# Kernel tuning notes

Hardware: AMD Instinct MI355X
Metric: run time of the kernel (lower is better)

The kernel has to match this reference:

```python
import jax, jax.numpy as jnp
import numpy as np

NEG_SLOPE = 0.2
NEG_INF = -1e9


def _gat_branch(x, src, dst, edge_type, t, W, a_src, a_dst, b):
    """Single-head PyG GATConv restricted (by masking) to edges with edge_type == t,
    with self-loops added (PyG default add_self_loops=True)."""
    N = x.shape[0]
    h = x @ W                                   # [N, out_dim]
    s = h @ a_src                               # [N] source attention term
    d = h @ a_dst                               # [N] destination attention term
    # real edges (masked by type)
    e_edge = jax.nn.leaky_relu(s[src] + d[dst], NEG_SLOPE)
    e_edge = jnp.where(edge_type == t, e_edge, NEG_INF)
    # self-loop edges i -> i
    e_self = jax.nn.leaky_relu(s + d, NEG_SLOPE)
    dst_all = jnp.concatenate([dst, jnp.arange(N)])          # [E+N]
    e_all = jnp.concatenate([e_edge, e_self])                 # [E+N]
    # softmax over incoming edges per destination node (segment softmax)
    m = jax.ops.segment_max(e_all, dst_all, num_segments=N)
    p = jnp.exp(e_all - m[dst_all])
    denom = jax.ops.segment_sum(p, dst_all, num_segments=N)
    alpha = p / denom[dst_all]                                 # [E+N]
    msg = jnp.concatenate([h[src], h], axis=0) * alpha[:, None]
    return jax.ops.segment_sum(msg, dst_all, num_segments=N) + b


def setup_inputs() -> dict:
    key = jax.random.key(0)
    ks = jax.random.split(key, 12)
    N, E, in_dim, out_dim = 100000, 1000000, 64, 64
    glorot = (6.0 / (in_dim + out_dim)) ** 0.5
    att = (6.0 / (1 + out_dim)) ** 0.5
    return {
        "x": jax.random.normal(ks[0], (N, in_dim), dtype=jnp.float32),
        "edge_index": jax.random.randint(ks[1], (2, E), 0, N),
        "edge_type": jax.random.randint(ks[2], (E,), 0, 2),
        "W_login": jax.random.uniform(ks[3], (in_dim, out_dim), jnp.float32, -glorot, glorot),
        "a_src_login": jax.random.uniform(ks[4], (out_dim,), jnp.float32, -att, att),
        "a_dst_login": jax.random.uniform(ks[5], (out_dim,), jnp.float32, -att, att),
        "b_login": jnp.zeros((out_dim,), jnp.float32),
        "W_exec": jax.random.uniform(ks[6], (in_dim, out_dim), jnp.float32, -glorot, glorot),
        "a_src_exec": jax.random.uniform(ks[7], (out_dim,), jnp.float32, -att, att),
        "a_dst_exec": jax.random.uniform(ks[8], (out_dim,), jnp.float32, -att, att),
        "b_exec": jnp.zeros((out_dim,), jnp.float32),
    }


def reference(x, edge_index, edge_type, W_login, a_src_login, a_dst_login, b_login,
              W_exec, a_src_exec, a_dst_exec, b_exec):
    src, dst = edge_index[0], edge_index[1]
    out = _gat_branch(x, src, dst, edge_type, 0, W_login, a_src_login, a_dst_login, b_login)
    out = out + _gat_branch(x, src, dst, edge_type, 1, W_exec, a_src_exec, a_dst_exec, b_exec)
    return out
```

## Files before the change

kernel.cpp:

```cpp
#include <hip/hip_runtime.h>

#define D 64
#define CAP 896
#define CNTB 512
#define GEMMB 768
#define BINCH 1600

typedef unsigned short u16;
typedef __attribute__((ext_vector_type(8))) __bf16 bf16x8;
typedef __attribute__((ext_vector_type(4))) float f32x4;

__device__ __forceinline__ float lrelu(float x) { return x > 0.f ? x : 0.2f * x; }
__device__ __forceinline__ u16 f2bf(float f) {
    unsigned u = __float_as_uint(f);
    return (u16)((u + 0x7fffu + ((u >> 16) & 1u)) >> 16);
}
__device__ __forceinline__ unsigned pack2(float lo, float hi) {
    return (unsigned)f2bf(lo) | ((unsigned)f2bf(hi) << 16);
}
__device__ __forceinline__ float blo(unsigned u) { return __uint_as_float(u << 16); }
__device__ __forceinline__ float bhi(unsigned u) { return __uint_as_float(u & 0xffff0000u); }

struct alignas(16) SG { u16 Xb[64][72]; float wsd[4][64]; };
struct SB { int cnt[BINCH]; };

__global__ __launch_bounds__(256) void k_wt(
    const float* __restrict__ W0, const float* __restrict__ as0, const float* __restrict__ ad0,
    const float* __restrict__ W1, const float* __restrict__ as1, const float* __restrict__ ad1,
    u16* __restrict__ Wt, float* __restrict__ wsd_g)
{
    const int tid = threadIdx.x;
    for (int i = tid; i < 4096; i += 256) {
        const int k = i >> 6, n = i & 63;
        Wt[(n << 6) + k]        = f2bf(W0[i]);
        Wt[4096 + (n << 6) + k] = f2bf(W1[i]);
    }
    const int k = tid & 63;
    const int v = tid >> 6;
    const float* Ws = (v < 2) ? W0 : W1;
    const float* av = (v == 0) ? as0 : (v == 1) ? ad0 : (v == 2) ? as1 : ad1;
    float q = 0.f;
    for (int n = 0; n < 64; ++n) q = fmaf(Ws[(k << 6) + n], av[n], q);
    wsd_g[(v << 6) + k] = q;
}

__global__ __launch_bounds__(256) void k_gc(
    const float* __restrict__ x,
    const u16* __restrict__ Wt, const float* __restrict__ wsd_g,
    u16* __restrict__ hb, float* __restrict__ s_tab, float* __restrict__ d_tab,
    int N, int ntiles,
    const int* __restrict__ dst, u16* __restrict__ cm, int E, int nbk, int Eseg)
{
    __shared__ union SM { SG g; SB bn; } sm;
    const int tid = threadIdx.x;

    if (blockIdx.x >= GEMMB) {
        int* cnt_l = sm.bn.cnt;
        const int blk = blockIdx.x - GEMMB;
        const long e0 = (long)blk * Eseg;
        const long e1 = min(e0 + (long)Eseg, (long)E);
        for (int base = 0; base < nbk; base += BINCH) {
            const int lim = min(BINCH, nbk - base);
            for (int i = tid; i < lim; i += 256) cnt_l[i] = 0;
            __syncthreads();
            long i = e0 + tid;
            for (; i + 256 * 7 < e1; i += 256 * 8) {
                int d8[8];
#pragma unroll
                for (int k = 0; k < 8; ++k) d8[k] = dst[i + 256 * k];
#pragma unroll
                for (int k = 0; k < 8; ++k) {
                    const int bb = (d8[k] >> 6) - base;
                    if ((unsigned)bb < (unsigned)lim) atomicAdd(&cnt_l[bb], 1);
                }
            }
            for (; i < e1; i += 256) {
                const int bb = (dst[i] >> 6) - base;
                if ((unsigned)bb < (unsigned)lim) atomicAdd(&cnt_l[bb], 1);
            }
            __syncthreads();
            for (int j = tid; j < lim; j += 256)
                cm[(size_t)(base + j) * CNTB + blk] = (u16)cnt_l[j];
            __syncthreads();
        }
        return;
    }

    auto& Xb  = sm.g.Xb;
    auto& wsd = sm.g.wsd;

    sm.g.wsd[tid >> 6][tid & 63] = wsd_g[tid];

    const int lane = tid & 63;
    const int nl = lane & 15, quad = lane >> 4;
    const int wv = tid >> 6;

    bf16x8 bfrag[2][4][2];
#pragma unroll
    for (int br = 0; br < 2; ++br)
#pragma unroll
        for (int t = 0; t < 4; ++t)
#pragma unroll
            for (int h = 0; h < 2; ++h)
                bfrag[br][t][h] = *(const bf16x8*)&Wt[((br << 12) | ((t * 16 + nl) << 6)) + h * 32 + quad * 8];

    __syncthreads();

    const int rstage = tid >> 2;
    const int kc = (tid & 3) << 4;

    for (int tile = blockIdx.x; tile < ntiles; tile += GEMMB) {
        const long n0 = (long)tile << 6;
        __syncthreads();
        {
            long row = n0 + rstage; if (row >= N) row = N - 1;
            const float4* xp = (const float4*)(x + row * D + kc);
            const float4 v0 = xp[0], v1 = xp[1], v2 = xp[2], v3 = xp[3];

            unsigned q[8];
            q[0] = pack2(v0.x, v0.y); q[1] = pack2(v0.z, v0.w);
            q[2] = pack2(v1.x, v1.y); q[3] = pack2(v1.z, v1.w);
            q[4] = pack2(v2.x, v2.y); q[5] = pack2(v2.z, v2.w);
            q[6] = pack2(v3.x, v3.y); q[7] = pack2(v3.z, v3.w);
            *(uint4*)&Xb[rstage][kc]     = make_uint4(q[0], q[1], q[2], q[3]);
            *(uint4*)&Xb[rstage][kc + 8] = make_uint4(q[4], q[5], q[6], q[7]);

            float ps[4];
#pragma unroll
            for (int v = 0; v < 4; ++v) {
                const float4* wp = (const float4*)&wsd[v][kc];
                const float4 wa = wp[0], wb = wp[1], wc = wp[2], wd = wp[3];
                float s = 0.f;
                s = fmaf(v0.x, wa.x, s); s = fmaf(v0.y, wa.y, s);
                s = fmaf(v0.z, wa.z, s); s = fmaf(v0.w, wa.w, s);
                s = fmaf(v1.x, wb.x, s); s = fmaf(v1.y, wb.y, s);
                s = fmaf(v1.z, wb.z, s); s = fmaf(v1.w, wb.w, s);
                s = fmaf(v2.x, wc.x, s); s = fmaf(v2.y, wc.y, s);
                s = fmaf(v2.z, wc.z, s); s = fmaf(v2.w, wc.w, s);
                s = fmaf(v3.x, wd.x, s); s = fmaf(v3.y, wd.y, s);
                s = fmaf(v3.z, wd.z, s); s = fmaf(v3.w, wd.w, s);
                ps[v] = s;
            }
#pragma unroll
            for (int v = 0; v < 4; ++v) {
                ps[v] += __shfl_xor(ps[v], 1, 64);
                ps[v] += __shfl_xor(ps[v], 2, 64);
            }
            const long rw = n0 + rstage;
            if ((tid & 3) == 0 && rw < N) {
                s_tab[(rw << 1)]     = ps[0]; d_tab[(rw << 1)]     = ps[1];
                s_tab[(rw << 1) | 1] = ps[2]; d_tab[(rw << 1) | 1] = ps[3];
            }
        }
        __syncthreads();

        const int rbase = wv << 4;
        const bf16x8 a0 = *(const bf16x8*)&Xb[rbase + nl][quad * 8];
        const bf16x8 a1 = *(const bf16x8*)&Xb[rbase + nl][32 + quad * 8];

        f32x4 acc[2][4];
#pragma unroll
        for (int br = 0; br < 2; ++br)
#pragma unroll
            for (int t = 0; t < 4; ++t) {
                f32x4 c = {0.f, 0.f, 0.f, 0.f};
                c = __builtin_amdgcn_mfma_f32_16x16x32_bf16(a0, bfrag[br][t][0], c, 0, 0, 0);
                c = __builtin_amdgcn_mfma_f32_16x16x32_bf16(a1, bfrag[br][t][1], c, 0, 0, 0);
                acc[br][t] = c;
            }

#pragma unroll
        for (int reg = 0; reg < 4; ++reg) {
            const long row = n0 + rbase + (quad << 2) + reg;
            if (row < N) {
#pragma unroll
                for (int br = 0; br < 2; ++br) {
                    uint2 v;
                    v.x = pack2(acc[br][0][reg], acc[br][1][reg]);
                    v.y = pack2(acc[br][2][reg], acc[br][3][reg]);
                    *(uint2*)(hb + (((row << 1) | br) << 6) + (nl << 2)) = v;
                }
            }
        }
    }
}

__global__ __launch_bounds__(256) void k_off(
    u16* __restrict__ cm, int* __restrict__ bktcnt, int nbk)
{
    const int lane = threadIdx.x & 63;
    const int j = blockIdx.x * 4 + (threadIdx.x >> 6);
    if (j >= nbk) return;

    const uint4 u = *(const uint4*)(cm + (size_t)j * CNTB + (lane << 3));
    int c[8] = { (int)(u.x & 0xffff), (int)(u.x >> 16),
                 (int)(u.y & 0xffff), (int)(u.y >> 16),
                 (int)(u.z & 0xffff), (int)(u.z >> 16),
                 (int)(u.w & 0xffff), (int)(u.w >> 16) };
    int e[8]; int run = 0;
#pragma unroll
    for (int k = 0; k < 8; ++k) { e[k] = run; run += c[k]; }
    int incl = run;
#pragma unroll
    for (int o = 1; o < 64; o <<= 1) {
        const int t = __shfl_up(incl, o, 64);
        if (lane >= o) incl += t;
    }
    const int excl = incl - run;
#pragma unroll
    for (int k = 0; k < 8; ++k) e[k] += excl;

    uint4 o4;
    o4.x = (unsigned)(e[0] & 0xffff) | ((unsigned)(e[1] & 0xffff) << 16);
    o4.y = (unsigned)(e[2] & 0xffff) | ((unsigned)(e[3] & 0xffff) << 16);
    o4.z = (unsigned)(e[4] & 0xffff) | ((unsigned)(e[5] & 0xffff) << 16);
    o4.w = (unsigned)(e[6] & 0xffff) | ((unsigned)(e[7] & 0xffff) << 16);
    *(uint4*)(cm + (size_t)j * CNTB + (lane << 3)) = o4;

    if (lane == 63) bktcnt[j] = incl;
}

__global__ __launch_bounds__(256) void k_emit(
    const int* __restrict__ src, const int* __restrict__ dst,
    const int* __restrict__ et, const u16* __restrict__ cm,
    unsigned* __restrict__ bkt, int E, int nbk, int Eseg)
{
    extern __shared__ int curl[];
    const int tid = threadIdx.x;
    const int blk = blockIdx.x;
    const long e0 = (long)blk * Eseg;
    const long e1 = min(e0 + (long)Eseg, (long)E);

    for (int base = 0; base < nbk; base += BINCH) {
        const int lim = min(BINCH, nbk - base);
        for (int i = tid; i < lim; i += 256)
            curl[i] = (int)cm[(size_t)(base + i) * CNTB + blk];
        __syncthreads();

        long i = e0 + tid;
        for (; i + 256 * 7 < e1; i += 256 * 8) {
            int d8[8], s8[8], t8[8];
#pragma unroll
            for (int k = 0; k < 8; ++k) d8[k] = dst[i + 256 * k];
#pragma unroll
            for (int k = 0; k < 8; ++k) s8[k] = src[i + 256 * k];
#pragma unroll
            for (int k = 0; k < 8; ++k) t8[k] = et[i + 256 * k];
#pragma unroll
            for (int k = 0; k < 8; ++k) {
                const int bb = (d8[k] >> 6) - base;
                if ((unsigned)bb < (unsigned)lim) {
                    const int slot = atomicAdd(&curl[bb], 1);
                    if (slot < CAP)
                        bkt[(long)(base + bb) * CAP + slot] =
                            ((unsigned)(d8[k] & 63) << 18) | ((unsigned)s8[k] << 1) | (unsigned)t8[k];
                }
            }
        }
        for (; i < e1; i += 256) {
            const int d = dst[i];
            const int bb = (d >> 6) - base;
            if ((unsigned)bb < (unsigned)lim) {
                const int slot = atomicAdd(&curl[bb], 1);
                if (slot < CAP)
                    bkt[(long)(base + bb) * CAP + slot] =
                        ((unsigned)(d & 63) << 18) | ((unsigned)src[i] << 1) | (unsigned)et[i];
            }
        }
        __syncthreads();
    }
}

__global__ __launch_bounds__(512) void k_proc(
    const int* __restrict__ bktcnt, const unsigned* __restrict__ bkt,
    const float* __restrict__ s_tab, const float* __restrict__ d_tab,
    const u16* __restrict__ hb,
    const float* __restrict__ b0, const float* __restrict__ b1,
    float* __restrict__ out, int N)
{
    __shared__ uint2 tok2[CAP + 128];
    __shared__ int   degl[64];
    __shared__ int   curl[64];
    __shared__ float den[128];
    __shared__ float dl[128];
    __shared__ float bsum[64];

    const int tid = threadIdx.x;
    const int b = blockIdx.x;
    const int lo = b << 6;
    const int cnt_nodes = min(64, N - lo);
    const int nb = min(bktcnt[b], CAP);

    if (tid < 64) {
        degl[tid] = (lo + tid < N) ? 2 : 0;
        bsum[tid] = b0[tid] + b1[tid];
    }
    if (tid < 128) {
        den[tid] = 0.f;
        const int n = lo + (tid >> 1);
        dl[tid] = (n < N) ? d_tab[(n << 1) | (tid & 1)] : 0.f;
    }
    __syncthreads();

    unsigned pr[2]; int ns = 0;
    for (int i = tid; i < nb; i += 512) {
        const unsigned p = bkt[(long)b * CAP + i];
        pr[ns++] = p;
        atomicAdd(&degl[(p >> 18) & 63], 1);
    }
    __syncthreads();
    if (tid < 64) {
        int v = degl[tid];
        const int orig = v;
#pragma unroll
        for (int o = 1; o < 64; o <<= 1) {
            const int u = __shfl_up(v, o, 64);
            if (tid >= o) v += u;
        }
        curl[tid] = v - orig;
    }
    __syncthreads();
    if (tid < 2 * cnt_nodes) {
        const int ni = tid >> 1;
        const int slot = atomicAdd(&curl[ni], 1);
        tok2[slot].x = ((unsigned)ni << 18) | ((unsigned)((lo + ni) << 1)) | (unsigned)(tid & 1);
    }
    for (int k = 0, i = tid; k < ns; i += 512, ++k) {
        const unsigned p = pr[k];
        const int slot = atomicAdd(&curl[(p >> 18) & 63], 1);
        tok2[slot].x = p;
    }
    __syncthreads();

    const int T = nb + (cnt_nodes << 1);
    for (int j = tid; j < T; j += 512) {
        const unsigned u = tok2[j].x;
        const int idx = (int)(((u >> 18) << 1) | (u & 1u));
        const float e = lrelu(s_tab[u & 0x3FFFFu] + dl[idx]);
        const float p = __expf(e);
        tok2[j].y = __float_as_uint(p);
        atomicAdd(&den[idx], p);
    }
    __syncthreads();

    const int lane = tid & 63;
    const int wave = tid >> 6;
    const int q = lane >> 4;
    const int cl = lane & 15;

    for (int ni = wave; ni < cnt_nodes; ni += 8) {
        const int cnt = degl[ni];
        const int off = curl[ni] - cnt;
        const float r0 = 1.f / den[(ni << 1)];
        const float r1 = 1.f / den[(ni << 1) | 1];

        float4 acc = {0.f, 0.f, 0.f, 0.f};
        const int nq = (cnt + 3) >> 2;
        int pp = 0;
        for (; pp + 1 < nq; pp += 2) {
            const int iA = (pp << 2) + q;
            const int iB = iA + 4;
            const uint2 eA = tok2[off + iA];
            const uint2 eB = tok2[off + (iB < cnt ? iB : cnt - 1)];
            const float aA = __uint_as_float(eA.y) * ((eA.x & 1u) ? r1 : r0);
            float aB = __uint_as_float(eB.y) * ((eB.x & 1u) ? r1 : r0);
            if (iB >= cnt) aB = 0.f;
            const uint2 uA = *(const uint2*)(hb + ((long)(eA.x & 0x3FFFFu) << 6) + (cl << 2));
            const uint2 uB = *(const uint2*)(hb + ((long)(eB.x & 0x3FFFFu) << 6) + (cl << 2));
            acc.x = fmaf(aA, blo(uA.x), acc.x);
            acc.y = fmaf(aA, bhi(uA.x), acc.y);
            acc.z = fmaf(aA, blo(uA.y), acc.z);
            acc.w = fmaf(aA, bhi(uA.y), acc.w);
            acc.x = fmaf(aB, blo(uB.x), acc.x);
            acc.y = fmaf(aB, bhi(uB.x), acc.y);
            acc.z = fmaf(aB, blo(uB.y), acc.z);
            acc.w = fmaf(aB, bhi(uB.y), acc.w);
        }
        if (pp < nq) {
            const int iA = (pp << 2) + q;
            const uint2 eA = tok2[off + (iA < cnt ? iA : cnt - 1)];
            float aA = __uint_as_float(eA.y) * ((eA.x & 1u) ? r1 : r0);
            if (iA >= cnt) aA = 0.f;
            const uint2 uA = *(const uint2*)(hb + ((long)(eA.x & 0x3FFFFu) << 6) + (cl << 2));
            acc.x = fmaf(aA, blo(uA.x), acc.x);
            acc.y = fmaf(aA, bhi(uA.x), acc.y);
            acc.z = fmaf(aA, blo(uA.y), acc.z);
            acc.w = fmaf(aA, bhi(uA.y), acc.w);
        }
        acc.x += __shfl_xor(acc.x, 16, 64);
        acc.y += __shfl_xor(acc.y, 16, 64);
        acc.z += __shfl_xor(acc.z, 16, 64);
        acc.w += __shfl_xor(acc.w, 16, 64);
        acc.x += __shfl_xor(acc.x, 32, 64);
        acc.y += __shfl_xor(acc.y, 32, 64);
        acc.z += __shfl_xor(acc.z, 32, 64);
        acc.w += __shfl_xor(acc.w, 32, 64);
        if (lane < 16) {
            float* op = out + ((long)(lo + ni) << 6);
            op[cl]      = acc.x + bsum[cl];
            op[16 + cl] = acc.y + bsum[16 + cl];
            op[32 + cl] = acc.z + bsum[32 + cl];
            op[48 + cl] = acc.w + bsum[48 + cl];
        }
    }
}

extern "C" void kernel_launch(void* const* d_in, const int* in_sizes, int n_in,
                              void* d_out, int out_size, void* d_ws, size_t ws_size,
                              hipStream_t stream) {
    const float* x   = (const float*)d_in[0];
    const int*   ei  = (const int*)d_in[1];
    const int*   et  = (const int*)d_in[2];
    const float* W0  = (const float*)d_in[3];
    const float* as0 = (const float*)d_in[4];
    const float* ad0 = (const float*)d_in[5];
    const float* b0  = (const float*)d_in[6];
    const float* W1  = (const float*)d_in[7];
    const float* as1 = (const float*)d_in[8];
    const float* ad1 = (const float*)d_in[9];
    const float* b1  = (const float*)d_in[10];
    float* out = (float*)d_out;

    const int N = in_sizes[0] / D;
    const int E = in_sizes[1] / 2;
    const int* src = ei;
    const int* dst = ei + E;

    const int nbk = (N + 63) >> 6;

    char* w = (char*)d_ws;
    auto carve = [&w](size_t bytes) {
        char* p = w;
        w += (bytes + 255) & ~(size_t)255;
        return p;
    };
    u16* hb       = (u16*)carve((size_t)2 * N * D * sizeof(u16));
    float* s_tab  = (float*)carve((size_t)2 * N * sizeof(float));
    float* d_tab  = (float*)carve((size_t)2 * N * sizeof(float));
    int* bktcnt   = (int*)carve((size_t)nbk * sizeof(int));
    unsigned* bkt = (unsigned*)carve((size_t)nbk * CAP * sizeof(unsigned));
    u16* cm       = (u16*)carve((size_t)nbk * CNTB * sizeof(u16));
    u16* Wt       = (u16*)carve((size_t)2 * 64 * 64 * sizeof(u16));
    float* wsd_g  = (float*)carve((size_t)4 * 64 * sizeof(float));

    const int ntiles = (N + 63) / 64;
    const int Eseg = (E + CNTB - 1) / CNTB;
    const int offb = (nbk + 3) / 4;

    k_wt<<<1, 256, 0, stream>>>(W0, as0, ad0, W1, as1, ad1, Wt, wsd_g);
    k_gc<<<GEMMB + CNTB, 256, 0, stream>>>(x, Wt, wsd_g,
                                           hb, s_tab, d_tab, N, ntiles,
                                           dst, cm, E, nbk, Eseg);
    k_off<<<offb, 256, 0, stream>>>(cm, bktcnt, nbk);
    k_emit<<<CNTB, 256, (size_t)BINCH * sizeof(int), stream>>>(
        src, dst, et, cm, bkt, E, nbk, Eseg);
    k_proc<<<nbk, 512, 0, stream>>>(bktcnt, bkt, s_tab, d_tab, hb, b0, b1, out, N);
}
```

Before: 185.0 us.

## Reschedule kernels: count first, overlap GEMM with bucket emit, prenormalize alphas

The weight-transpose work moves into the histogram-count kernel as an extra block, and the prefix-offset kernel now runs before the GEMM. The bucket-emit phase is then co-scheduled with the GEMM blocks in one launch, instead of the count phase sharing the launch with the GEMM. This removes one launch and overlaps the heavier scatter work with the dense matmul. In the aggregation kernel, the per-token alpha is multiplied by the reciprocal denominator in a shared-memory pass, so the inner loop no longer selects per branch. The trade-off is an extra sync and shared-memory pass per block, and the count kernel now runs alone without overlap.

```diff
diff --git a/kernel.cpp b/kernel.cpp
--- a/kernel.cpp
+++ b/kernel.cpp
@@ -22,65 +22,149 @@
 __device__ __forceinline__ float bhi(unsigned u) { return __uint_as_float(u & 0xffff0000u); }
 
 struct alignas(16) SG { u16 Xb[64][72]; float wsd[4][64]; };
-struct SB { int cnt[BINCH]; };
-
-__global__ __launch_bounds__(256) void k_wt(
+
+__global__ __launch_bounds__(256) void k_cnt(
+    const int* __restrict__ dst, u16* __restrict__ cm, int E, int nbk, int Eseg,
     const float* __restrict__ W0, const float* __restrict__ as0, const float* __restrict__ ad0,
     const float* __restrict__ W1, const float* __restrict__ as1, const float* __restrict__ ad1,
     u16* __restrict__ Wt, float* __restrict__ wsd_g)
 {
+    __shared__ int cnt_l[BINCH];
     const int tid = threadIdx.x;
-    for (int i = tid; i < 4096; i += 256) {
-        const int k = i >> 6, n = i & 63;
-        Wt[(n << 6) + k]        = f2bf(W0[i]);
-        Wt[4096 + (n << 6) + k] = f2bf(W1[i]);
-    }
-    const int k = tid & 63;
-    const int v = tid >> 6;
-    const float* Ws = (v < 2) ? W0 : W1;
-    const float* av = (v == 0) ? as0 : (v == 1) ? ad0 : (v == 2) ? as1 : ad1;
-    float q = 0.f;
-    for (int n = 0; n < 64; ++n) q = fmaf(Ws[(k << 6) + n], av[n], q);
-    wsd_g[(v << 6) + k] = q;
-}
-
-__global__ __launch_bounds__(256) void k_gc(
+
+    if (blockIdx.x >= CNTB) {
+        for (int i = tid; i < 4096; i += 256) {
+            const int k = i >> 6, n = i & 63;
+            Wt[(n << 6) + k]        = f2bf(W0[i]);
+            Wt[4096 + (n << 6) + k] = f2bf(W1[i]);
+        }
+        const int k = tid & 63;
+        const int v = tid >> 6;
+        const float* Ws = (v < 2) ? W0 : W1;
+        const float* av = (v == 0) ? as0 : (v == 1) ? ad0 : (v == 2) ? as1 : ad1;
+        float q = 0.f;
+        for (int n = 0; n < 64; ++n) q = fmaf(Ws[(k << 6) + n], av[n], q);
+        wsd_g[(v << 6) + k] = q;
+        return;
+    }
+
+    const int blk = blockIdx.x;
+    const long e0 = (long)blk * Eseg;
+    const long e1 = min(e0 + (long)Eseg, (long)E);
+    for (int base = 0; base < nbk; base += BINCH) {
+        const int lim = min(BINCH, nbk - base);
+        for (int i = tid; i < lim; i += 256) cnt_l[i] = 0;
+        __syncthreads();
+        long i = e0 + tid;
+        for (; i + 256 * 7 < e1; i += 256 * 8) {
+            int d8[8];
+#pragma unroll
+            for (int k = 0; k < 8; ++k) d8[k] = dst[i + 256 * k];
+#pragma unroll
+            for (int k = 0; k < 8; ++k) {
+                const int bb = (d8[k] >> 6) - base;
+                if ((unsigned)bb < (unsigned)lim) atomicAdd(&cnt_l[bb], 1);
+            }
+        }
+        for (; i < e1; i += 256) {
+            const int bb = (dst[i] >> 6) - base;
+            if ((unsigned)bb < (unsigned)lim) atomicAdd(&cnt_l[bb], 1);
+        }
+        __syncthreads();
+        for (int j = tid; j < lim; j += 256)
+            cm[(size_t)(base + j) * CNTB + blk] = (u16)cnt_l[j];
+        __syncthreads();
+    }
+}
+
+__global__ __launch_bounds__(256) void k_off(
+    u16* __restrict__ cm, int* __restrict__ bktcnt, int nbk)
+{
+    const int lane = threadIdx.x & 63;
+    const int j = blockIdx.x * 4 + (threadIdx.x >> 6);
+    if (j >= nbk) return;
+
+    const uint4 u = *(const uint4*)(cm + (size_t)j * CNTB + (lane << 3));
+    int c[8] = { (int)(u.x & 0xffff), (int)(u.x >> 16),
+                 (int)(u.y & 0xffff), (int)(u.y >> 16),
+                 (int)(u.z & 0xffff), (int)(u.z >> 16),
+                 (int)(u.w & 0xffff), (int)(u.w >> 16) };
+    int e[8]; int run = 0;
+#pragma unroll
+    for (int k = 0; k < 8; ++k) { e[k] = run; run += c[k]; }
+    int incl = run;
+#pragma unroll
+    for (int o = 1; o < 64; o <<= 1) {
+        const int t = __shfl_up(incl, o, 64);
+        if (lane >= o) incl += t;
+    }
+    const int excl = incl - run;
+#pragma unroll
+    for (int k = 0; k < 8; ++k) e[k] += excl;
+
+    uint4 o4;
+    o4.x = (unsigned)(e[0] & 0xffff) | ((unsigned)(e[1] & 0xffff) << 16);
+    o4.y = (unsigned)(e[2] & 0xffff) | ((unsigned)(e[3] & 0xffff) << 16);
+    o4.z = (unsigned)(e[4] & 0xffff) | ((unsigned)(e[5] & 0xffff) << 16);
+    o4.w = (unsigned)(e[6] & 0xffff) | ((unsigned)(e[7] & 0xffff) << 16);
+    *(uint4*)(cm + (size_t)j * CNTB + (lane << 3)) = o4;
+
+    if (lane == 63) bktcnt[j] = incl;
+}
+
+__global__ __launch_bounds__(256) void k_ge(
     const float* __restrict__ x,
     const u16* __restrict__ Wt, const float* __restrict__ wsd_g,
     u16* __restrict__ hb, float* __restrict__ s_tab, float* __restrict__ d_tab,
     int N, int ntiles,
-    const int* __restrict__ dst, u16* __restrict__ cm, int E, int nbk, int Eseg)
+    const int* __restrict__ src, const int* __restrict__ dst, const int* __restrict__ et,
+    const u16* __restrict__ cm, unsigned* __restrict__ bkt, int E, int nbk, int Eseg)
 {
-    __shared__ union SM { SG g; SB bn; } sm;
+    __shared__ union SM { SG g; int cnt[BINCH]; } sm;
     const int tid = threadIdx.x;
 
     if (blockIdx.x >= GEMMB) {
-        int* cnt_l = sm.bn.cnt;
+        int* curl = sm.cnt;
         const int blk = blockIdx.x - GEMMB;
         const long e0 = (long)blk * Eseg;
         const long e1 = min(e0 + (long)Eseg, (long)E);
+
         for (int base = 0; base < nbk; base += BINCH) {
             const int lim = min(BINCH, nbk - base);
-            for (int i = tid; i < lim; i += 256) cnt_l[i] = 0;
+            for (int i = tid; i < lim; i += 256)
+                curl[i] = (int)cm[(size_t)(base + i) * CNTB + blk];
             __syncthreads();
+
             long i = e0 + tid;
             for (; i + 256 * 7 < e1; i += 256 * 8) {
-                int d8[8];
+                int d8[8], s8[8], t8[8];
 #pragma unroll
                 for (int k = 0; k < 8; ++k) d8[k] = dst[i + 256 * k];
+#pragma unroll
+                for (int k = 0; k < 8; ++k) s8[k] = src[i + 256 * k];
+#pragma unroll
+                for (int k = 0; k < 8; ++k) t8[k] = et[i + 256 * k];
 #pragma unroll
                 for (int k = 0; k < 8; ++k) {
                     const int bb = (d8[k] >> 6) - base;
-                    if ((unsigned)bb < (unsigned)lim) atomicAdd(&cnt_l[bb], 1);
+                    if ((unsigned)bb < (unsigned)lim) {
+                        const int slot = atomicAdd(&curl[bb], 1);
+                        if (slot < CAP)
+                            bkt[(long)(base + bb) * CAP + slot] =
+                                ((unsigned)(d8[k] & 63) << 18) | ((unsigned)s8[k] << 1) | (unsigned)t8[k];
+                    }
                 }
             }
             for (; i < e1; i += 256) {
-                const int bb = (dst[i] >> 6) - base;
-                if ((unsigned)bb < (unsigned)lim) atomicAdd(&cnt_l[bb], 1);
-            }
-            __syncthreads();
-            for (int j = tid; j < lim; j += 256)
-                cm[(size_t)(base + j) * CNTB + blk] = (u16)cnt_l[j];
+                const int d = dst[i];
+                const int bb = (d >> 6) - base;
+                if ((unsigned)bb < (unsigned)lim) {
+                    const int slot = atomicAdd(&curl[bb], 1);
+                    if (slot < CAP)
+                        bkt[(long)(base + bb) * CAP + slot] =
+                            ((unsigned)(d & 63) << 18) | ((unsigned)src[i] << 1) | (unsigned)et[i];
+                }
+            }
             __syncthreads();
         }
         return;
@@ -185,92 +269,6 @@
     }
 }
 
-__global__ __launch_bounds__(256) void k_off(
-    u16* __restrict__ cm, int* __restrict__ bktcnt, int nbk)
-{
-    const int lane = threadIdx.x & 63;
-    const int j = blockIdx.x * 4 + (threadIdx.x >> 6);
-    if (j >= nbk) return;
-
-    const uint4 u = *(const uint4*)(cm + (size_t)j * CNTB + (lane << 3));
-    int c[8] = { (int)(u.x & 0xffff), (int)(u.x >> 16),
-                 (int)(u.y & 0xffff), (int)(u.y >> 16),
-                 (int)(u.z & 0xffff), (int)(u.z >> 16),
-                 (int)(u.w & 0xffff), (int)(u.w >> 16) };
-    int e[8]; int run = 0;
-#pragma unroll
-    for (int k = 0; k < 8; ++k) { e[k] = run; run += c[k]; }
-    int incl = run;
-#pragma unroll
-    for (int o = 1; o < 64; o <<= 1) {
-        const int t = __shfl_up(incl, o, 64);
-        if (lane >= o) incl += t;
-    }
-    const int excl = incl - run;
-#pragma unroll
-    for (int k = 0; k < 8; ++k) e[k] += excl;
-
-    uint4 o4;
-    o4.x = (unsigned)(e[0] & 0xffff) | ((unsigned)(e[1] & 0xffff) << 16);
-    o4.y = (unsigned)(e[2] & 0xffff) | ((unsigned)(e[3] & 0xffff) << 16);
-    o4.z = (unsigned)(e[4] & 0xffff) | ((unsigned)(e[5] & 0xffff) << 16);
-    o4.w = (unsigned)(e[6] & 0xffff) | ((unsigned)(e[7] & 0xffff) << 16);
-    *(uint4*)(cm + (size_t)j * CNTB + (lane << 3)) = o4;
-
-    if (lane == 63) bktcnt[j] = incl;
-}
-
-__global__ __launch_bounds__(256) void k_emit(
-    const int* __restrict__ src, const int* __restrict__ dst,
-    const int* __restrict__ et, const u16* __restrict__ cm,
-    unsigned* __restrict__ bkt, int E, int nbk, int Eseg)
-{
-    extern __shared__ int curl[];
-    const int tid = threadIdx.x;
-    const int blk = blockIdx.x;
-    const long e0 = (long)blk * Eseg;
-    const long e1 = min(e0 + (long)Eseg, (long)E);
-
-    for (int base = 0; base < nbk; base += BINCH) {
-        const int lim = min(BINCH, nbk - base);
-        for (int i = tid; i < lim; i += 256)
-            curl[i] = (int)cm[(size_t)(base + i) * CNTB + blk];
-        __syncthreads();
-
-        long i = e0 + tid;
-        for (; i + 256 * 7 < e1; i += 256 * 8) {
-            int d8[8], s8[8], t8[8];
-#pragma unroll
-            for (int k = 0; k < 8; ++k) d8[k] = dst[i + 256 * k];
-#pragma unroll
-            for (int k = 0; k < 8; ++k) s8[k] = src[i + 256 * k];
-#pragma unroll
-            for (int k = 0; k < 8; ++k) t8[k] = et[i + 256 * k];
-#pragma unroll
-            for (int k = 0; k < 8; ++k) {
-                const int bb = (d8[k] >> 6) - base;
-                if ((unsigned)bb < (unsigned)lim) {
-                    const int slot = atomicAdd(&curl[bb], 1);
-                    if (slot < CAP)
-                        bkt[(long)(base + bb) * CAP + slot] =
-                            ((unsigned)(d8[k] & 63) << 18) | ((unsigned)s8[k] << 1) | (unsigned)t8[k];
-                }
-            }
-        }
-        for (; i < e1; i += 256) {
-            const int d = dst[i];
-            const int bb = (d >> 6) - base;
-            if ((unsigned)bb < (unsigned)lim) {
-                const int slot = atomicAdd(&curl[bb], 1);
-                if (slot < CAP)
-                    bkt[(long)(base + bb) * CAP + slot] =
-                        ((unsigned)(d & 63) << 18) | ((unsigned)src[i] << 1) | (unsigned)et[i];
-            }
-        }
-        __syncthreads();
-    }
-}
-
 __global__ __launch_bounds__(512) void k_proc(
     const int* __restrict__ bktcnt, const unsigned* __restrict__ bkt,
     const float* __restrict__ s_tab, const float* __restrict__ d_tab,
@@ -343,6 +341,15 @@
     }
     __syncthreads();
 
+    if (tid < 128) den[tid] = 1.f / den[tid];
+    __syncthreads();
+    for (int j = tid; j < T; j += 512) {
+        const unsigned u = tok2[j].x;
+        const int idx = (int)(((u >> 18) << 1) | (u & 1u));
+        tok2[j].y = __float_as_uint(__uint_as_float(tok2[j].y) * den[idx]);
+    }
+    __syncthreads();
+
     const int lane = tid & 63;
     const int wave = tid >> 6;
     const int q = lane >> 4;
@@ -351,8 +358,6 @@
     for (int ni = wave; ni < cnt_nodes; ni += 8) {
         const int cnt = degl[ni];
         const int off = curl[ni] - cnt;
-        const float r0 = 1.f / den[(ni << 1)];
-        const float r1 = 1.f / den[(ni << 1) | 1];
 
         float4 acc = {0.f, 0.f, 0.f, 0.f};
         const int nq = (cnt + 3) >> 2;
@@ -362,8 +367,8 @@
             const int iB = iA + 4;
             const uint2 eA = tok2[off + iA];
             const uint2 eB = tok2[off + (iB < cnt ? iB : cnt - 1)];
-            const float aA = __uint_as_float(eA.y) * ((eA.x & 1u) ? r1 : r0);
-            float aB = __uint_as_float(eB.y) * ((eB.x & 1u) ? r1 : r0);
+            const float aA = __uint_as_float(eA.y);
+            float aB = __uint_as_float(eB.y);
             if (iB >= cnt) aB = 0.f;
             const uint2 uA = *(const uint2*)(hb + ((long)(eA.x & 0x3FFFFu) << 6) + (cl << 2));
             const uint2 uB = *(const uint2*)(hb + ((long)(eB.x & 0x3FFFFu) << 6) + (cl << 2));
@@ -379,7 +384,7 @@
         if (pp < nq) {
             const int iA = (pp << 2) + q;
             const uint2 eA = tok2[off + (iA < cnt ? iA : cnt - 1)];
-            float aA = __uint_as_float(eA.y) * ((eA.x & 1u) ? r1 : r0);
+            float aA = __uint_as_float(eA.y);
             if (iA >= cnt) aA = 0.f;
             const uint2 uA = *(const uint2*)(hb + ((long)(eA.x & 0x3FFFFu) << 6) + (cl << 2));
             acc.x = fmaf(aA, blo(uA.x), acc.x);
@@ -447,12 +452,11 @@
     const int Eseg = (E + CNTB - 1) / CNTB;
     const int offb = (nbk + 3) / 4;
 
-    k_wt<<<1, 256, 0, stream>>>(W0, as0, ad0, W1, as1, ad1, Wt, wsd_g);
-    k_gc<<<GEMMB + CNTB, 256, 0, stream>>>(x, Wt, wsd_g,
+    k_cnt<<<CNTB + 1, 256, 0, stream>>>(dst, cm, E, nbk, Eseg,
+                                        W0, as0, ad0, W1, as1, ad1, Wt, wsd_g);
+    k_off<<<offb, 256, 0, stream>>>(cm, bktcnt, nbk);
+    k_ge<<<GEMMB + CNTB, 256, 0, stream>>>(x, Wt, wsd_g,
                                            hb, s_tab, d_tab, N, ntiles,
-                                           dst, cm, E, nbk, Eseg);
-    k_off<<<offb, 256, 0, stream>>>(cm, bktcnt, nbk);
-    k_emit<<<CNTB, 256, (size_t)BINCH * sizeof(int), stream>>>(
-        src, dst, et, cm, bkt, E, nbk, Eseg);
+                                           src, dst, et, cm, bkt, E, nbk, Eseg);
     k_proc<<<nbk, 512, 0, stream>>>(bktcnt, bkt, s_tab, d_tab, hb, b0, b1, out, N);
 }
```

After: 174.6 us. 1.06x faster.
